# Kernel tuning notes

Hardware: AMD Instinct MI355X
Metric: run time of the kernel (lower is better)

Reference implementation:

```python
import jax, jax.numpy as jnp
import numpy as np

VOCAB = 32000
EMB = 32
HID = 16
SEQ = 128
BATCH = 32


def setup_inputs() -> dict:
    key = jax.random.key(0)
    ks = jax.random.split(key, 7)
    stdv = 1.0 / np.sqrt(HID)
    u = lambda k, shape: jax.random.uniform(k, shape, jnp.float32, -stdv, stdv)
    return {
        "input_batch": jax.random.randint(ks[0], (SEQ, BATCH), 0, VOCAB),
        "h0": jax.random.normal(ks[1], (BATCH, HID), jnp.float32),
        "embedding": u(ks[2], (VOCAB, EMB)),
        "W_ih": u(ks[3], (HID, EMB + HID)),
        "b_ih": u(ks[4], (HID,)),
        "W_ho": u(ks[5], (VOCAB, HID)),
        "b_ho": u(ks[6], (VOCAB,)),
    }


def reference(input_batch, h0, embedding, W_ih, b_ih, W_ho, b_ho):
    # Embedding lookup for all timesteps: [S, B, EMB]
    emb_seq = embedding[input_batch]

    def step(h, x_t):
        # Torch code detaches both input and hidden before the cell (.data)
        combined = jax.lax.stop_gradient(jnp.concatenate([x_t, h], axis=1))  # [B, EMB+HID]
        h_new = jnp.tanh(combined @ W_ih.T + b_ih)                           # [B, HID]
        logits = h_new @ W_ho.T + b_ho                                       # [B, VOCAB]
        out = jax.nn.log_softmax(logits, axis=-1)
        return h_new, out

    _, predictions = jax.lax.scan(step, h0, emb_seq)  # [S, B, VOCAB]
    return predictions
```

## Files before the change

kernel.cpp:

```cpp
#include <hip/hip_runtime.h>
#include <math.h>

#define VOCAB 32000
#define EMB   32
#define HID   16
#define SEQ   128
#define BATCH 32
#define ROWS  (SEQ*BATCH)
#define WIH_LD (EMB+HID)
#define VBLK  2048
#define NVB   16
#define RCH   128
#define NRC   32

__global__ __launch_bounds__(128) void k_embed(const int* __restrict__ tok,
    const float* __restrict__ emb, const float* __restrict__ Wih,
    const float* __restrict__ bih, float* __restrict__ X)
{
    __shared__ float sW[HID][EMB];
    __shared__ float sb[HID];
    int t = threadIdx.x;
    for (int i = t; i < HID*EMB; i += 128)
        sW[i/EMB][i%EMB] = Wih[(i/EMB)*WIH_LD + (i%EMB)];
    if (t < HID) sb[t] = bih[t];
    __syncthreads();

    int row = blockIdx.x*128 + t;
    int token = tok[row];
    float x[EMB];
    const float4* ep = (const float4*)(emb + (long)token*EMB);
    #pragma unroll
    for (int q = 0; q < EMB/4; ++q) {
        float4 v = ep[q];
        x[4*q+0]=v.x; x[4*q+1]=v.y; x[4*q+2]=v.z; x[4*q+3]=v.w;
    }
    #pragma unroll
    for (int j = 0; j < HID; ++j) {
        float acc = sb[j];
        #pragma unroll
        for (int e = 0; e < EMB; ++e) acc = fmaf(sW[j][e], x[e], acc);
        X[row*HID + j] = acc;
    }
}

__global__ __launch_bounds__(512) void k_rnn(const float* __restrict__ X,
    const float* __restrict__ h0, const float* __restrict__ Wih,
    float* __restrict__ H)
{
    __shared__ float sWh[HID][HID];
    __shared__ float h[2][BATCH][HID];
    int t = threadIdx.x;
    if (t < HID*HID)
        sWh[t/HID][t%HID] = Wih[(t/HID)*WIH_LD + EMB + (t%HID)];
    h[0][t>>4][t&15] = h0[t];
    __syncthreads();

    int b = t >> 4, j = t & 15;
    int cur = 0;
    float x = X[t];
    for (int s = 0; s < SEQ; ++s) {
        float xn = (s+1 < SEQ) ? X[(s+1)*512 + t] : 0.f;
        float acc = x;
        #pragma unroll
        for (int k = 0; k < HID; ++k) acc = fmaf(sWh[j][k], h[cur][b][k], acc);
        float e2 = __expf(fminf(2.f*acc, 30.f));
        float hn = (e2 - 1.f) / (e2 + 1.f);
        h[cur^1][b][j] = hn;
        H[s*512 + t] = hn;
        __syncthreads();
        x = xn; cur ^= 1;
    }
}

__global__ __launch_bounds__(256, 2) void k_sumexp(const float* __restrict__ Who,
    const float* __restrict__ bho, const float* __restrict__ H,
    float* __restrict__ part)
{
    int t = threadIdx.x;
    int vblk = blockIdx.x;
    float w[2][4][HID]; float bb[2][4];
    #pragma unroll
    for (int g = 0; g < 2; ++g) {
        int base = vblk*VBLK + g*1024 + 4*t;
        #pragma unroll
        for (int c = 0; c < 4; ++c) {
            int v = base + c;
            if (v < VOCAB) {
                const float4* wp = (const float4*)(Who + (long)v*HID);
                #pragma unroll
                for (int q = 0; q < 4; ++q) {
                    float4 f = wp[q];
                    w[g][c][4*q+0]=f.x; w[g][c][4*q+1]=f.y;
                    w[g][c][4*q+2]=f.z; w[g][c][4*q+3]=f.w;
                }
                bb[g][c] = bho[v];
            } else {
                #pragma unroll
                for (int i = 0; i < HID; ++i) w[g][c][i] = 0.f;
                bb[g][c] = -1e30f;
            }
        }
    }

    int wid = t >> 6, lane = t & 63;
    for (int r = 0; r < RCH; r += 2) {
        int row0 = blockIdx.y*RCH + r;
        float h0[HID], h1[HID];
        const float4* hp0 = (const float4*)(H + row0*HID);
        const float4* hp1 = (const float4*)(H + (row0+1)*HID);
        #pragma unroll
        for (int q = 0; q < 4; ++q) {
            float4 f0 = hp0[q], f1 = hp1[q];
            h0[4*q+0]=f0.x; h0[4*q+1]=f0.y; h0[4*q+2]=f0.z; h0[4*q+3]=f0.w;
            h1[4*q+0]=f1.x; h1[4*q+1]=f1.y; h1[4*q+2]=f1.z; h1[4*q+3]=f1.w;
        }
        float p0 = 0.f, p1 = 0.f;
        #pragma unroll
        for (int g = 0; g < 2; ++g)
        #pragma unroll
        for (int c = 0; c < 4; ++c) {
            float a0 = bb[g][c], a1 = bb[g][c];
            #pragma unroll
            for (int i = 0; i < HID; ++i) {
                a0 = fmaf(w[g][c][i], h0[i], a0);
                a1 = fmaf(w[g][c][i], h1[i], a1);
            }
            p0 += __expf(a0);
            p1 += __expf(a1);
        }
        #pragma unroll
        for (int off = 32; off > 0; off >>= 1) {
            p0 += __shfl_xor(p0, off, 64);
            p1 += __shfl_xor(p1, off, 64);
        }
        if (lane == 0) {
            part[(long)row0*64     + vblk*4 + wid] = p0;
            part[(long)(row0+1)*64 + vblk*4 + wid] = p1;
        }
    }
}

__global__ __launch_bounds__(256) void k_logl(const float* __restrict__ part,
    float* __restrict__ logl)
{
    int t = threadIdx.x;
    int row = blockIdx.x*4 + (t>>6);
    int lane = t & 63;
    float p = part[row*64 + lane];
    #pragma unroll
    for (int off = 32; off > 0; off >>= 1) p += __shfl_xor(p, off, 64);
    if (lane == 0) logl[row] = logf(p);
}

__global__ __launch_bounds__(256, 2) void k_write(const float* __restrict__ Who,
    const float* __restrict__ bho, const float* __restrict__ H,
    const float* __restrict__ logl, float* __restrict__ out)
{
    int t = threadIdx.x;
    int vblk = blockIdx.x;
    float w[2][4][HID]; float bb[2][4];
    #pragma unroll
    for (int g = 0; g < 2; ++g) {
        int base = vblk*VBLK + g*1024 + 4*t;
        #pragma unroll
        for (int c = 0; c < 4; ++c) {
            int v = base + c;
            if (v < VOCAB) {
                const float4* wp = (const float4*)(Who + (long)v*HID);
                #pragma unroll
                for (int q = 0; q < 4; ++q) {
                    float4 f = wp[q];
                    w[g][c][4*q+0]=f.x; w[g][c][4*q+1]=f.y;
                    w[g][c][4*q+2]=f.z; w[g][c][4*q+3]=f.w;
                }
                bb[g][c] = bho[v];
            } else {
                #pragma unroll
                for (int i = 0; i < HID; ++i) w[g][c][i] = 0.f;
                bb[g][c] = 0.f;
            }
        }
    }

    for (int r = 0; r < RCH; ++r) {
        int row = blockIdx.y*RCH + r;
        float h[HID];
        const float4* hp = (const float4*)(H + row*HID);
        #pragma unroll
        for (int q = 0; q < 4; ++q) {
            float4 f = hp[q];
            h[4*q+0]=f.x; h[4*q+1]=f.y; h[4*q+2]=f.z; h[4*q+3]=f.w;
        }
        float ll = logl[row];
        float* orow = out + (long)row*VOCAB;
        #pragma unroll
        for (int g = 0; g < 2; ++g) {
            int base = vblk*VBLK + g*1024 + 4*t;
            float acc[4];
            #pragma unroll
            for (int c = 0; c < 4; ++c) {
                float a = bb[g][c];
                #pragma unroll
                for (int i = 0; i < HID; ++i) a = fmaf(w[g][c][i], h[i], a);
                acc[c] = a - ll;
            }
            if (base < VOCAB) {
                float4 o; o.x=acc[0]; o.y=acc[1]; o.z=acc[2]; o.w=acc[3];
                *(float4*)(orow + base) = o;
            }
        }
    }
}

extern "C" void kernel_launch(void* const* d_in, const int* in_sizes, int n_in,
                              void* d_out, int out_size, void* d_ws, size_t ws_size,
                              hipStream_t stream)
{
    const int*   tok = (const int*)  d_in[0];
    const float* h0  = (const float*)d_in[1];
    const float* emb = (const float*)d_in[2];
    const float* Wih = (const float*)d_in[3];
    const float* bih = (const float*)d_in[4];
    const float* Who = (const float*)d_in[5];
    const float* bho = (const float*)d_in[6];
    float* out = (float*)d_out;

    char* ws = (char*)d_ws;
    float* X    = (float*)(ws);
    float* H    = (float*)(ws + 262144);
    float* part = (float*)(ws + 524288);
    float* logl = (float*)(ws + 1572864);

    k_embed <<<dim3(ROWS/128), 128, 0, stream>>>(tok, emb, Wih, bih, X);
    k_rnn   <<<dim3(1), 512, 0, stream>>>(X, h0, Wih, H);
    k_sumexp<<<dim3(NVB, NRC), 256, 0, stream>>>(Who, bho, H, part);
    k_logl  <<<dim3(ROWS/4), 256, 0, stream>>>(part, logl);
    k_write <<<dim3(NVB, NRC), 256, 0, stream>>>(Who, bho, H, logl, out);
}
```

Measured before the change: 712.6 us.

## Fuse all stages into one persistent kernel with atomic flag pipelining

Merges the embed, RNN, sum-exp, log-normalizer and write kernels into a single 512-block kernel that coordinates through global atomic counters and flags. Block 0 runs the serial recurrence and publishes a ready flag every 4 timesteps, so the vocab blocks for each 128-row group can begin sum-exp work while later timesteps are still being computed. The last block to finish each group computes the log-normalizers, which removes the separate reduction kernel. W_ho stays in registers across both passes instead of being reloaded by a second kernel. This relies on all 512 blocks being co-resident at once and adds spin-wait loops with timeout breaks.

```diff
diff --git a/kernel.cpp b/kernel.cpp
--- a/kernel.cpp
+++ b/kernel.cpp
@@ -9,75 +9,46 @@
 #define ROWS  (SEQ*BATCH)
 #define WIH_LD (EMB+HID)
 #define VBLK  2048
-#define NVB   16
-#define RCH   128
-#define NRC   32
-
-__global__ __launch_bounds__(128) void k_embed(const int* __restrict__ tok,
+#define AGENT __HIP_MEMORY_SCOPE_AGENT
+
+
+__global__ __launch_bounds__(256, 2) void k_fused(
+    const int* __restrict__ tok, const float* __restrict__ h0f,
     const float* __restrict__ emb, const float* __restrict__ Wih,
-    const float* __restrict__ bih, float* __restrict__ X)
-{
-    __shared__ float sW[HID][EMB];
-    __shared__ float sb[HID];
-    int t = threadIdx.x;
-    for (int i = t; i < HID*EMB; i += 128)
-        sW[i/EMB][i%EMB] = Wih[(i/EMB)*WIH_LD + (i%EMB)];
-    if (t < HID) sb[t] = bih[t];
-    __syncthreads();
-
-    int row = blockIdx.x*128 + t;
-    int token = tok[row];
-    float x[EMB];
-    const float4* ep = (const float4*)(emb + (long)token*EMB);
-    #pragma unroll
-    for (int q = 0; q < EMB/4; ++q) {
-        float4 v = ep[q];
-        x[4*q+0]=v.x; x[4*q+1]=v.y; x[4*q+2]=v.z; x[4*q+3]=v.w;
-    }
-    #pragma unroll
-    for (int j = 0; j < HID; ++j) {
-        float acc = sb[j];
-        #pragma unroll
-        for (int e = 0; e < EMB; ++e) acc = fmaf(sW[j][e], x[e], acc);
-        X[row*HID + j] = acc;
-    }
-}
-
-__global__ __launch_bounds__(512) void k_rnn(const float* __restrict__ X,
-    const float* __restrict__ h0, const float* __restrict__ Wih,
-    float* __restrict__ H)
+    const float* __restrict__ bih, const float* __restrict__ Who,
+    const float* __restrict__ bho,
+    float* __restrict__ X, float* __restrict__ H,
+    float* __restrict__ part, float* __restrict__ logl,
+    unsigned* __restrict__ sync_, float* __restrict__ out)
 {
     __shared__ float sWh[HID][HID];
-    __shared__ float h[2][BATCH][HID];
-    int t = threadIdx.x;
-    if (t < HID*HID)
-        sWh[t/HID][t%HID] = Wih[(t/HID)*WIH_LD + EMB + (t%HID)];
-    h[0][t>>4][t&15] = h0[t];
-    __syncthreads();
-
-    int b = t >> 4, j = t & 15;
-    int cur = 0;
-    float x = X[t];
-    for (int s = 0; s < SEQ; ++s) {
-        float xn = (s+1 < SEQ) ? X[(s+1)*512 + t] : 0.f;
-        float acc = x;
-        #pragma unroll
-        for (int k = 0; k < HID; ++k) acc = fmaf(sWh[j][k], h[cur][b][k], acc);
-        float e2 = __expf(fminf(2.f*acc, 30.f));
-        float hn = (e2 - 1.f) / (e2 + 1.f);
-        h[cur^1][b][j] = hn;
-        H[s*512 + t] = hn;
-        __syncthreads();
-        x = xn; cur ^= 1;
-    }
-}
-
-__global__ __launch_bounds__(256, 2) void k_sumexp(const float* __restrict__ Who,
-    const float* __restrict__ bho, const float* __restrict__ H,
-    float* __restrict__ part)
-{
-    int t = threadIdx.x;
-    int vblk = blockIdx.x;
+    __shared__ float hh[2][BATCH][HID];
+    __shared__ unsigned srank;
+    int t = threadIdx.x, bid = blockIdx.x;
+
+    int gtid = bid*256 + t;
+    if (gtid < ROWS*HID) {
+        int row = gtid >> 4, j = gtid & 15;
+        int token = tok[row];
+        const float4* ep = (const float4*)(emb + (long)token*EMB);
+        const float4* wp = (const float4*)(Wih + j*WIH_LD);
+        float acc = bih[j];
+        #pragma unroll
+        for (int q = 0; q < 8; ++q) {
+            float4 e = ep[q], wv = wp[q];
+            acc = fmaf(wv.x, e.x, acc); acc = fmaf(wv.y, e.y, acc);
+            acc = fmaf(wv.z, e.z, acc); acc = fmaf(wv.w, e.w, acc);
+        }
+        X[gtid] = acc;
+    }
+    __syncthreads();
+    if (t == 0) {
+        __threadfence();
+        __hip_atomic_fetch_add(&sync_[0], 1u, __ATOMIC_ACQ_REL, AGENT);
+    }
+
+    int sid  = (bid == 0) ? 511 : bid - 1;
+    int vblk = sid & 15, grp = sid >> 4;
     float w[2][4][HID]; float bb[2][4];
     #pragma unroll
     for (int g = 0; g < 2; ++g) {
@@ -86,10 +57,10 @@
         for (int c = 0; c < 4; ++c) {
             int v = base + c;
             if (v < VOCAB) {
-                const float4* wp = (const float4*)(Who + (long)v*HID);
+                const float4* qp = (const float4*)(Who + (long)v*HID);
                 #pragma unroll
                 for (int q = 0; q < 4; ++q) {
-                    float4 f = wp[q];
+                    float4 f = qp[q];
                     w[g][c][4*q+0]=f.x; w[g][c][4*q+1]=f.y;
                     w[g][c][4*q+2]=f.z; w[g][c][4*q+3]=f.w;
                 }
@@ -102,9 +73,67 @@
         }
     }
 
+    if (bid == 0) {
+        if (t < HID*HID)
+            sWh[t/HID][t%HID] = Wih[(t/HID)*WIH_LD + EMB + (t%HID)];
+        hh[0][t>>4][t&15]        = h0f[t];
+        hh[0][16 + (t>>4)][t&15] = h0f[t + 256];
+        if (t == 0) {
+            long gcnt = 0;
+            while (__hip_atomic_load(&sync_[0], __ATOMIC_RELAXED, AGENT) < 512u) {
+                __builtin_amdgcn_s_sleep(2);
+                if (++gcnt > (1L<<23)) break;
+            }
+            __threadfence();
+        }
+        __syncthreads();
+
+        __builtin_amdgcn_s_setprio(1);
+        int b0 = t >> 4, j = t & 15;
+        int cur = 0;
+        float x0 = X[t], x1 = X[t + 256];
+        for (int s = 0; s < SEQ; ++s) {
+            float xn0 = (s+1 < SEQ) ? X[(s+1)*512 + t]       : 0.f;
+            float xn1 = (s+1 < SEQ) ? X[(s+1)*512 + t + 256] : 0.f;
+            float a0 = x0, a1 = x1;
+            #pragma unroll
+            for (int k = 0; k < HID; ++k) {
+                float wv = sWh[j][k];
+                a0 = fmaf(wv, hh[cur][b0][k],      a0);
+                a1 = fmaf(wv, hh[cur][b0+16][k],   a1);
+            }
+            float e0 = __expf(fminf(2.f*a0, 30.f));
+            float e1 = __expf(fminf(2.f*a1, 30.f));
+            float hn0 = (e0 - 1.f) / (e0 + 1.f);
+            float hn1 = (e1 - 1.f) / (e1 + 1.f);
+            hh[cur^1][b0][j]    = hn0;
+            hh[cur^1][b0+16][j] = hn1;
+            H[s*512 + t]       = hn0;
+            H[s*512 + t + 256] = hn1;
+            __syncthreads();
+            if ((s & 3) == 3 && t == 0) {
+                __threadfence();
+                __hip_atomic_store(&sync_[16 + (s>>2)*16], 1u,
+                                   __ATOMIC_RELEASE, AGENT);
+            }
+            x0 = xn0; x1 = xn1; cur ^= 1;
+        }
+        __builtin_amdgcn_s_setprio(0);
+    }
+
+    if (t == 0) {
+        long gcnt = 0;
+        while (__hip_atomic_load(&sync_[16 + grp*16], __ATOMIC_RELAXED, AGENT) == 0u) {
+            __builtin_amdgcn_s_sleep(2);
+            if (++gcnt > (1L<<23)) break;
+        }
+        __threadfence();
+    }
+    __syncthreads();
+
     int wid = t >> 6, lane = t & 63;
-    for (int r = 0; r < RCH; r += 2) {
-        int row0 = blockIdx.y*RCH + r;
+    for (int r = 0; r < 128; r += 2) {
+        int row0 = grp*128 + r;
         float h0[HID], h1[HID];
         const float4* hp0 = (const float4*)(H + row0*HID);
         const float4* hp1 = (const float4*)(H + (row0+1)*HID);
@@ -138,52 +167,43 @@
             part[(long)(row0+1)*64 + vblk*4 + wid] = p1;
         }
     }
-}
-
-__global__ __launch_bounds__(256) void k_logl(const float* __restrict__ part,
-    float* __restrict__ logl)
-{
-    int t = threadIdx.x;
-    int row = blockIdx.x*4 + (t>>6);
-    int lane = t & 63;
-    float p = part[row*64 + lane];
-    #pragma unroll
-    for (int off = 32; off > 0; off >>= 1) p += __shfl_xor(p, off, 64);
-    if (lane == 0) logl[row] = logf(p);
-}
-
-__global__ __launch_bounds__(256, 2) void k_write(const float* __restrict__ Who,
-    const float* __restrict__ bho, const float* __restrict__ H,
-    const float* __restrict__ logl, float* __restrict__ out)
-{
-    int t = threadIdx.x;
-    int vblk = blockIdx.x;
-    float w[2][4][HID]; float bb[2][4];
-    #pragma unroll
-    for (int g = 0; g < 2; ++g) {
-        int base = vblk*VBLK + g*1024 + 4*t;
-        #pragma unroll
-        for (int c = 0; c < 4; ++c) {
-            int v = base + c;
-            if (v < VOCAB) {
-                const float4* wp = (const float4*)(Who + (long)v*HID);
-                #pragma unroll
-                for (int q = 0; q < 4; ++q) {
-                    float4 f = wp[q];
-                    w[g][c][4*q+0]=f.x; w[g][c][4*q+1]=f.y;
-                    w[g][c][4*q+2]=f.z; w[g][c][4*q+3]=f.w;
-                }
-                bb[g][c] = bho[v];
-            } else {
-                #pragma unroll
-                for (int i = 0; i < HID; ++i) w[g][c][i] = 0.f;
-                bb[g][c] = 0.f;
-            }
-        }
-    }
-
-    for (int r = 0; r < RCH; ++r) {
-        int row = blockIdx.y*RCH + r;
+    __syncthreads();
+    if (t == 0) {
+        __threadfence();
+        srank = __hip_atomic_fetch_add(&sync_[528 + grp*16], 1u,
+                                       __ATOMIC_ACQ_REL, AGENT);
+    }
+    __syncthreads();
+
+    if (srank == 15u) {
+        if (t == 0) __threadfence();
+        __syncthreads();
+        for (int rr = 0; rr < 32; ++rr) {
+            int row = grp*128 + wid*32 + rr;
+            float p = part[(long)row*64 + lane];
+            #pragma unroll
+            for (int off = 32; off > 0; off >>= 1) p += __shfl_xor(p, off, 64);
+            if (lane == 0) logl[row] = logf(p);
+        }
+        __syncthreads();
+        if (t == 0) {
+            __threadfence();
+            __hip_atomic_store(&sync_[1040 + grp*16], 1u,
+                               __ATOMIC_RELEASE, AGENT);
+        }
+    }
+    if (t == 0) {
+        long gcnt = 0;
+        while (__hip_atomic_load(&sync_[1040 + grp*16], __ATOMIC_RELAXED, AGENT) == 0u) {
+            __builtin_amdgcn_s_sleep(2);
+            if (++gcnt > (1L<<23)) break;
+        }
+        __threadfence();
+    }
+    __syncthreads();
+
+    for (int r = 0; r < 128; ++r) {
+        int row = grp*128 + r;
         float h[HID];
         const float4* hp = (const float4*)(H + row*HID);
         #pragma unroll
@@ -226,14 +246,13 @@
     float* out = (float*)d_out;
 
     char* ws = (char*)d_ws;
-    float* X    = (float*)(ws);
-    float* H    = (float*)(ws + 262144);
-    float* part = (float*)(ws + 524288);
-    float* logl = (float*)(ws + 1572864);
-
-    k_embed <<<dim3(ROWS/128), 128, 0, stream>>>(tok, emb, Wih, bih, X);
-    k_rnn   <<<dim3(1), 512, 0, stream>>>(X, h0, Wih, H);
-    k_sumexp<<<dim3(NVB, NRC), 256, 0, stream>>>(Who, bho, H, part);
-    k_logl  <<<dim3(ROWS/4), 256, 0, stream>>>(part, logl);
-    k_write <<<dim3(NVB, NRC), 256, 0, stream>>>(Who, bho, H, logl, out);
+    float*    X    = (float*)(ws);
+    float*    H    = (float*)(ws + 262144);
+    float*    part = (float*)(ws + 524288);
+    float*    logl = (float*)(ws + 1572864);
+    unsigned* sync_ = (unsigned*)(ws + 1589248);
+
+    hipMemsetAsync(sync_, 0, 8192, stream);
+    k_fused<<<dim3(512), 256, 0, stream>>>(tok, h0, emb, Wih, bih, Who, bho,
+                                           X, H, part, logl, sync_, out);
 }
```

Measured after the change: 786.1 us. 1.1x slower.
